# Performance work log

Measured on AMD Instinct MI355X. Metric: run time of the kernel, lower is better.

The kernel has to match this reference:

```python
import jax, jax.numpy as jnp
import numpy as np

SPARSITY = 5      # sparsity_level
DIAG_EPS = 1e-6   # max(epsilon, 1e-6) regularizer on gram_active
NORM_EPS = 1e-10  # epsilon used for atom normalization


def setup_inputs() -> dict:
    key = jax.random.key(0)
    kx, kd = jax.random.split(key)
    M, N, B = 64, 512, 65536
    X = jax.random.normal(kx, (M, B), dtype=jnp.float32)
    D = jax.random.normal(kd, (M, N), dtype=jnp.float32)
    # normalize_atoms=True: unit-L2 columns
    D = D / (jnp.linalg.norm(D, axis=0, keepdims=True) + NORM_EPS)
    return {"X": X, "D": D}


def reference(X, D):
    """Batched Orthogonal Matching Pursuit (KSVDDictionaryLearning.batch_omp).

    X: (M, B) signals, D: (M, N) column-normalized dictionary.
    Returns sparse coefficients (N, B) with SPARSITY nonzeros per column.
    """
    M, B = X.shape
    N = D.shape[1]
    gram = D.T @ D            # (N, N)
    dt_x_t = (D.T @ X).T      # (B, N)
    coeff = jnp.zeros((N, B), X.dtype)
    mask = jnp.zeros((N, B), dtype=bool)
    batch_idx = jnp.arange(B)
    selected = []
    for k in range(SPARSITY):  # fixed small unroll; active-set size grows k+1
        residual = X - D @ coeff                  # (M, B)
        corr = D.T @ residual                     # (N, B)
        corr = jnp.where(mask, 0.0, corr)
        idx = jnp.argmax(jnp.abs(corr), axis=0)   # (B,)
        selected.append(idx)
        mask = mask.at[idx, batch_idx].set(True)
        active = jnp.stack(selected, axis=1)      # (B, k+1)
        # gram restricted to active atoms: (B, k+1, k+1)
        gram_active = gram[active[:, :, None], active[:, None, :]]
        gram_active = gram_active + DIAG_EPS * jnp.eye(k + 1, dtype=gram.dtype)
        rhs = jnp.take_along_axis(dt_x_t, active, axis=1)          # (B, k+1)
        sol = jnp.linalg.solve(gram_active, rhs[..., None])[..., 0]  # (B, k+1)
        # rebuild coefficients: active covers every atom selected so far,
        # so scattering solutions into zeros matches the torch in-place writes
        coeff = jnp.zeros((N, B), X.dtype).at[active.T, batch_idx[None, :]].set(sol.T)
    return coeff
```

## Files before the change

kernel.cpp:

```cpp
#include <hip/hip_runtime.h>
#include <math.h>

#define NATOMS  512
#define MROWS   64
#define BATCH   65536
#define BT      4
#define NSPARSE 5
#define DEPSF   1e-6f

__global__ void ksvd_prep(const float* __restrict__ D,
                          float* __restrict__ gram) {
  const int idx = blockIdx.x * 256 + threadIdx.x;
  const int i = idx >> 9;
  const int j = idx & (NATOMS - 1);
  double acc = 0.0;
#pragma unroll 8
  for (int m = 0; m < MROWS; ++m)
    acc += (double)D[m * NATOMS + i] * (double)D[m * NATOMS + j];
  gram[idx] = (float)acc;
}

__device__ __forceinline__ float wave_max_nonneg(float x) {
  int v = __builtin_bit_cast(int, x);
#define DPP_MAX_STEP(ctrl)                                                   \
  {                                                                          \
    const int t = __builtin_amdgcn_update_dpp(0, v, (ctrl), 0xf, 0xf, true); \
    v = __builtin_bit_cast(                                                  \
        int, fmaxf(__builtin_bit_cast(float, v), __builtin_bit_cast(float, t))); \
  }
  DPP_MAX_STEP(0x111)
  DPP_MAX_STEP(0x112)
  DPP_MAX_STEP(0x114)
  DPP_MAX_STEP(0x118)
  DPP_MAX_STEP(0x142)
  DPP_MAX_STEP(0x143)
#undef DPP_MAX_STEP
  return __builtin_bit_cast(float, __builtin_amdgcn_readlane(v, 63));
}

__device__ __forceinline__ float readlane_f(float v, int l) {
  return __builtin_bit_cast(float,
      __builtin_amdgcn_readlane(__builtin_bit_cast(int, v), l));
}

__global__ __launch_bounds__(512, 2) void ksvd_main(
    const float* __restrict__ X, const float* __restrict__ D,
    const float* __restrict__ gram, float* __restrict__ out) {
  __shared__ union {
    float4 xs4[MROWS];
    float  dtxT[BT][NATOMS];
  } sh;
  __shared__ float exv[BT][NSPARSE][2];
  __shared__ int   exn[BT][NSPARSE][2];
  __shared__ float exd[BT][NSPARSE][2];

  const int t    = threadIdx.x;
  const int lane = t & 63;
  const int w    = t >> 6;
  const int cw   = w >> 1;
  const int h    = w & 1;
  const int b0   = blockIdx.x * BT;

  if (t < MROWS)
    sh.xs4[t] = *reinterpret_cast<const float4*>(&X[(size_t)t * BATCH + b0]);
  __syncthreads();

  const int aw = 64 * w + lane;
  float accA[BT], accB[BT];
#pragma unroll
  for (int c = 0; c < BT; ++c) { accA[c] = 0.f; accB[c] = 0.f; }

#pragma unroll 4
  for (int m = 0; m < MROWS; m += 2) {
    const float dA = D[m * NATOMS + aw];
    const float dB = D[(m + 1) * NATOMS + aw];
    const float4 xa = sh.xs4[m];
    const float4 xb = sh.xs4[m + 1];
    accA[0] = fmaf(dA, xa.x, accA[0]); accB[0] = fmaf(dB, xb.x, accB[0]);
    accA[1] = fmaf(dA, xa.y, accA[1]); accB[1] = fmaf(dB, xb.y, accB[1]);
    accA[2] = fmaf(dA, xa.z, accA[2]); accB[2] = fmaf(dB, xb.z, accB[2]);
    accA[3] = fmaf(dA, xa.w, accA[3]); accB[3] = fmaf(dB, xb.w, accB[3]);
  }
  __syncthreads();
#pragma unroll
  for (int c = 0; c < BT; ++c)
    sh.dtxT[c][aw] = accA[c] + accB[c];
  __syncthreads();

  const int cglob = b0 + cw;
  float dtxr[4];
  {
    const float4 f =
        *reinterpret_cast<const float4*>(&sh.dtxT[cw][256 * h + 4 * lane]);
    dtxr[0] = f.x; dtxr[1] = f.y; dtxr[2] = f.z; dtxr[3] = f.w;
  }

  int   idxs[NSPARSE];
  float gc[NSPARSE - 1][4];
  float L[NSPARSE][NSPARSE];
  float inv_d[NSPARSE];
  float y[NSPARSE];
  float sol[NSPARSE];

#pragma unroll
  for (int k = 0; k < NSPARSE; ++k) {
    float bv   = -1.0f;
    int   bn   = 0;
    float bdtx = 0.0f;
#pragma unroll
    for (int jj = 0; jj < 4; ++jj) {
      float cv = dtxr[jj];
#pragma unroll
      for (int s = 0; s < k; ++s) cv -= sol[s] * gc[s][jj];
      const float av = fabsf(cv);
      if (av > bv) { bv = av; bn = 256 * h + 4 * lane + jj; bdtx = dtxr[jj]; }
    }
    const float wmax = wave_max_nonneg(bv);
    const unsigned long long own = __ballot(bv == wmax);
    const int owner = __ffsll((long long)own) - 1;
    int   widx = __builtin_amdgcn_readlane(bn, owner);
    float wdtx = readlane_f(bdtx, owner);
    widx = __builtin_amdgcn_readfirstlane(widx);

    if (lane == 0) {
      exv[cw][k][h] = wmax; exn[cw][k][h] = widx; exd[cw][k][h] = wdtx;
    }
    __syncthreads();
    const float v0 = exv[cw][k][0], v1 = exv[cw][k][1];
    const bool take0 = (v0 >= v1);
    int idx = take0 ? exn[cw][k][0] : exn[cw][k][1];
    const float rhsk = take0 ? exd[cw][k][0] : exd[cw][k][1];
    idx = __builtin_amdgcn_readfirstlane(idx);
    idxs[k] = idx;

    if (k < NSPARSE - 1) {
      const float4 g = *reinterpret_cast<const float4*>(
          &gram[(size_t)idx * NATOMS + 256 * h + 4 * lane]);
      gc[k][0] = g.x; gc[k][1] = g.y; gc[k][2] = g.z; gc[k][3] = g.w;
    }

    float arowf[NSPARSE];
#pragma unroll
    for (int j = 0; j < k; ++j)
      arowf[j] = gram[(size_t)idx * NATOMS + idxs[j]];
    const float gdiag = gram[(size_t)idx * NATOMS + idx];

    float ss = gdiag + DEPSF;
#pragma unroll
    for (int j = 0; j < k; ++j) {
      float ww = arowf[j];
#pragma unroll
      for (int tt = 0; tt < j; ++tt) ww -= L[k][tt] * L[j][tt];
      ww *= inv_d[j];
      L[k][j] = ww;
      ss -= ww * ww;
    }
    const float inv = rsqrtf(ss);
    L[k][k]  = ss * inv;
    inv_d[k] = inv;

    {
      float s2 = rhsk;
#pragma unroll
      for (int j = 0; j < k; ++j) s2 -= L[k][j] * y[j];
      y[k] = s2 * inv;
    }
#pragma unroll
    for (int i = k; i >= 0; --i) {
      float s2 = y[i];
#pragma unroll
      for (int j = i + 1; j <= k; ++j) s2 -= L[j][i] * sol[j];
      sol[i] = s2 * inv_d[i];
    }
  }

  if (h == 0 && lane == 0) {
#pragma unroll
    for (int s = 0; s < NSPARSE; ++s)
      out[(size_t)idxs[s] * BATCH + cglob] = sol[s];
  }
}

extern "C" void kernel_launch(void* const* d_in, const int* in_sizes, int n_in,
                              void* d_out, int out_size, void* d_ws,
                              size_t ws_size, hipStream_t stream) {
  (void)in_sizes; (void)n_in; (void)out_size; (void)ws_size;
  const float* X = (const float*)d_in[0];
  const float* D = (const float*)d_in[1];
  float* out = (float*)d_out;
  float* gram = (float*)d_ws;

  ksvd_prep<<<(NATOMS * NATOMS) / 256, 256, 0, stream>>>(D, gram);
  hipMemsetAsync(out, 0, (size_t)NATOMS * BATCH * sizeof(float), stream);
  ksvd_main<<<BATCH / BT, 512, 0, stream>>>(X, D, gram, out);
}
```

Before: 191.3 us.

## Pack D^T X projection into v2f FMAs and share Cholesky solve via LDS

The D^T X projection now runs on four waves, each lane handling two atoms with packed two-wide FMAs on pre-duplicated X values staged in LDS. The per-step Cholesky solve now runs only in the h==0 wave, which passes the solution to its partner wave through shared memory after an extra barrier. The aim is to cut redundant scalar FMA work and duplicated solve work, at the cost of one more block-wide sync per sparsity step and half the waves sitting idle during the projection.

```diff
diff --git a/kernel.cpp b/kernel.cpp
--- a/kernel.cpp
+++ b/kernel.cpp
@@ -7,6 +7,8 @@
 #define BT      4
 #define NSPARSE 5
 #define DEPSF   1e-6f
+
+typedef float v2f __attribute__((ext_vector_type(2)));
 
 __global__ void ksvd_prep(const float* __restrict__ D,
                           float* __restrict__ gram) {
@@ -47,12 +49,13 @@
     const float* __restrict__ X, const float* __restrict__ D,
     const float* __restrict__ gram, float* __restrict__ out) {
   __shared__ union {
-    float4 xs4[MROWS];
+    float4 xs4[MROWS][2];
     float  dtxT[BT][NATOMS];
   } sh;
   __shared__ float exv[BT][NSPARSE][2];
   __shared__ int   exn[BT][NSPARSE][2];
   __shared__ float exd[BT][NSPARSE][2];
+  __shared__ float solX[BT][NSPARSE];
 
   const int t    = threadIdx.x;
   const int lane = t & 63;
@@ -61,30 +64,50 @@
   const int h    = w & 1;
   const int b0   = blockIdx.x * BT;
 
-  if (t < MROWS)
-    sh.xs4[t] = *reinterpret_cast<const float4*>(&X[(size_t)t * BATCH + b0]);
+  if (t < MROWS * 2) {
+    const int m = t >> 1, p = t & 1;
+    const float x0 = X[(size_t)m * BATCH + b0 + 2 * p];
+    const float x1 = X[(size_t)m * BATCH + b0 + 2 * p + 1];
+    float4 v; v.x = x0; v.y = x0; v.z = x1; v.w = x1;
+    sh.xs4[m][p] = v;
+  }
   __syncthreads();
 
-  const int aw = 64 * w + lane;
-  float accA[BT], accB[BT];
-#pragma unroll
-  for (int c = 0; c < BT; ++c) { accA[c] = 0.f; accB[c] = 0.f; }
-
+  if (w < 4) {
+    const int a0 = w * 128 + 2 * lane;
+    v2f accA[BT], accB[BT];
+#pragma unroll
+    for (int c = 0; c < BT; ++c) {
+      accA[c].x = 0.f; accA[c].y = 0.f;
+      accB[c].x = 0.f; accB[c].y = 0.f;
+    }
 #pragma unroll 4
-  for (int m = 0; m < MROWS; m += 2) {
-    const float dA = D[m * NATOMS + aw];
-    const float dB = D[(m + 1) * NATOMS + aw];
-    const float4 xa = sh.xs4[m];
-    const float4 xb = sh.xs4[m + 1];
-    accA[0] = fmaf(dA, xa.x, accA[0]); accB[0] = fmaf(dB, xb.x, accB[0]);
-    accA[1] = fmaf(dA, xa.y, accA[1]); accB[1] = fmaf(dB, xb.y, accB[1]);
-    accA[2] = fmaf(dA, xa.z, accA[2]); accB[2] = fmaf(dB, xb.z, accB[2]);
-    accA[3] = fmaf(dA, xa.w, accA[3]); accB[3] = fmaf(dB, xb.w, accB[3]);
-  }
-  __syncthreads();
-#pragma unroll
-  for (int c = 0; c < BT; ++c)
-    sh.dtxT[c][aw] = accA[c] + accB[c];
+    for (int m = 0; m < MROWS; m += 2) {
+      const v2f dA = *reinterpret_cast<const v2f*>(&D[m * NATOMS + a0]);
+      const v2f dB = *reinterpret_cast<const v2f*>(&D[(m + 1) * NATOMS + a0]);
+      const float4 xa0 = sh.xs4[m][0];
+      const float4 xa1 = sh.xs4[m][1];
+      const float4 xb0 = sh.xs4[m + 1][0];
+      const float4 xb1 = sh.xs4[m + 1][1];
+      v2f xv;
+      xv.x = xa0.x; xv.y = xa0.y; accA[0] = __builtin_elementwise_fma(dA, xv, accA[0]);
+      xv.x = xa0.z; xv.y = xa0.w; accA[1] = __builtin_elementwise_fma(dA, xv, accA[1]);
+      xv.x = xa1.x; xv.y = xa1.y; accA[2] = __builtin_elementwise_fma(dA, xv, accA[2]);
+      xv.x = xa1.z; xv.y = xa1.w; accA[3] = __builtin_elementwise_fma(dA, xv, accA[3]);
+      xv.x = xb0.x; xv.y = xb0.y; accB[0] = __builtin_elementwise_fma(dB, xv, accB[0]);
+      xv.x = xb0.z; xv.y = xb0.w; accB[1] = __builtin_elementwise_fma(dB, xv, accB[1]);
+      xv.x = xb1.x; xv.y = xb1.y; accB[2] = __builtin_elementwise_fma(dB, xv, accB[2]);
+      xv.x = xb1.z; xv.y = xb1.w; accB[3] = __builtin_elementwise_fma(dB, xv, accB[3]);
+    }
+    __syncthreads();
+#pragma unroll
+    for (int c = 0; c < BT; ++c) {
+      const v2f s = accA[c] + accB[c];
+      *reinterpret_cast<v2f*>(&sh.dtxT[c][a0]) = s;
+    }
+  } else {
+    __syncthreads();
+  }
   __syncthreads();
 
   const int cglob = b0 + cw;
@@ -139,38 +162,49 @@
       gc[k][0] = g.x; gc[k][1] = g.y; gc[k][2] = g.z; gc[k][3] = g.w;
     }
 
-    float arowf[NSPARSE];
-#pragma unroll
-    for (int j = 0; j < k; ++j)
-      arowf[j] = gram[(size_t)idx * NATOMS + idxs[j]];
-    const float gdiag = gram[(size_t)idx * NATOMS + idx];
-
-    float ss = gdiag + DEPSF;
-#pragma unroll
-    for (int j = 0; j < k; ++j) {
-      float ww = arowf[j];
-#pragma unroll
-      for (int tt = 0; tt < j; ++tt) ww -= L[k][tt] * L[j][tt];
-      ww *= inv_d[j];
-      L[k][j] = ww;
-      ss -= ww * ww;
-    }
-    const float inv = rsqrtf(ss);
-    L[k][k]  = ss * inv;
-    inv_d[k] = inv;
-
-    {
-      float s2 = rhsk;
-#pragma unroll
-      for (int j = 0; j < k; ++j) s2 -= L[k][j] * y[j];
-      y[k] = s2 * inv;
-    }
-#pragma unroll
-    for (int i = k; i >= 0; --i) {
-      float s2 = y[i];
-#pragma unroll
-      for (int j = i + 1; j <= k; ++j) s2 -= L[j][i] * sol[j];
-      sol[i] = s2 * inv_d[i];
+    if (h == 0) {
+      float arowf[NSPARSE];
+#pragma unroll
+      for (int j = 0; j < k; ++j)
+        arowf[j] = gram[(size_t)idx * NATOMS + idxs[j]];
+      const float gdiag = gram[(size_t)idx * NATOMS + idx];
+
+      float ss = gdiag + DEPSF;
+#pragma unroll
+      for (int j = 0; j < k; ++j) {
+        float ww = arowf[j];
+#pragma unroll
+        for (int tt = 0; tt < j; ++tt) ww -= L[k][tt] * L[j][tt];
+        ww *= inv_d[j];
+        L[k][j] = ww;
+        ss -= ww * ww;
+      }
+      const float inv = rsqrtf(ss);
+      L[k][k]  = ss * inv;
+      inv_d[k] = inv;
+
+      {
+        float s2 = rhsk;
+#pragma unroll
+        for (int j = 0; j < k; ++j) s2 -= L[k][j] * y[j];
+        y[k] = s2 * inv;
+      }
+#pragma unroll
+      for (int i = k; i >= 0; --i) {
+        float s2 = y[i];
+#pragma unroll
+        for (int j = i + 1; j <= k; ++j) s2 -= L[j][i] * sol[j];
+        sol[i] = s2 * inv_d[i];
+      }
+      if (lane == 0) {
+#pragma unroll
+        for (int s = 0; s <= k; ++s) solX[cw][s] = sol[s];
+      }
+    }
+    __syncthreads();
+    if (h == 1) {
+#pragma unroll
+      for (int s = 0; s <= k; ++s) sol[s] = solX[cw][s];
     }
   }
 
```

Result: slower. 230.7 us (+20.6%).
